# Kernel tuning notes

Measured on AMD Instinct MI355X. Metric: run time of the kernel, lower is better.

The kernel has to match this reference:

```python
import jax, jax.numpy as jnp
import numpy as np

KEY_BITS = 1024
VALUE_BITS = 1024
CAPACITY = 65536
BATCH = 2048


def setup_inputs() -> dict:
    key = jax.random.key(0)
    kq, kk, kv = jax.random.split(key, 3)
    query = jax.random.randint(kq, (BATCH, KEY_BITS), 0, 2, dtype=jnp.int32)
    keys = jax.random.randint(kk, (CAPACITY, KEY_BITS), 0, 2, dtype=jnp.int32)
    values = jax.random.normal(kv, (CAPACITY, VALUE_BITS), dtype=jnp.float32)
    return {"query": query, "keys": keys, "values": values}


def reference(query, keys, values):
    # Hamming mismatches between 0/1 bit vectors via GEMM:
    #   popcount(q ^ k) = sum(q) + sum(k) - 2 * (q . k)
    qf = query.astype(jnp.float32)                      # [B, key_bits]
    kf = keys.astype(jnp.float32)                       # [C, key_bits]
    dot = jnp.einsum('bk,ck->bc', qf, kf)               # [B, C]
    mismatches = qf.sum(axis=1, keepdims=True) + kf.sum(axis=1)[None, :] - 2.0 * dot
    sim = KEY_BITS - mismatches                         # similarity = key_bits - Hamming dist
    best_idx = jnp.argmax(sim, axis=1)                  # first max, matches strict '>' loop
    return values[best_idx]                             # [B, value_bits]
```

## Files before the change

### kernel.cpp

```cpp
#include <hip/hip_runtime.h>
#include <stdint.h>

typedef int v4i  __attribute__((ext_vector_type(4)));
typedef int v16i __attribute__((ext_vector_type(16)));

#define CAPACITY  65536
#define BATCH     2048
#define KBITS     1024
#define NSTEP     16
#define NBUF      3


__global__ void prep_i8_kernel(const int* __restrict__ in,
                               unsigned char* __restrict__ out8,
                               int* __restrict__ sums) {
    const int row = blockIdx.x, t = threadIdx.x;
    int4 v = reinterpret_cast<const int4*>(in)[(size_t)row * 256 + t];
    uint32_t b = (uint32_t)(v.x & 1)        | ((uint32_t)(v.y & 1) << 8) |
                 ((uint32_t)(v.z & 1) << 16) | ((uint32_t)(v.w & 1) << 24);
    reinterpret_cast<uint32_t*>(out8)[(size_t)row * 256 + t] = b;
    int s = (v.x & 1) + (v.y & 1) + (v.z & 1) + (v.w & 1);
    for (int off = 32; off; off >>= 1) s += __shfl_xor(s, off, 64);
    __shared__ int ws4[4];
    if ((t & 63) == 0) ws4[t >> 6] = s;
    __syncthreads();
    if (t == 0) sums[row] = ws4[0] + ws4[1] + ws4[2] + ws4[3];
}

__global__ void init_best_kernel(uint32_t* __restrict__ best) {
    best[blockIdx.x * 256 + threadIdx.x] = 0xFFFFFFFFu;
}

__device__ __forceinline__ int swz(int idx) { return idx ^ ((idx >> 3) & 7); }

__launch_bounds__(256, 2)
__global__ void gemm_scan_kernel(const unsigned char* __restrict__ qi8,
                                 const unsigned char* __restrict__ ki8,
                                 const int* __restrict__ sumk,
                                 uint32_t* __restrict__ best) {
    __shared__ uint4 sA[NBUF][512];
    __shared__ uint4 sB[NBUF][1024];

    const int t    = threadIdx.x;
    const int lane = t & 63, wid = t >> 6;
    const int wr   = wid >> 1, wc = wid & 1;
    const int ln   = lane & 31, kh = lane >> 5;

    const int b     = blockIdx.x;
    const int slot  = b >> 3;
    const int ntile = (b & 7) * 32 + (slot >> 4);
    const int mtile = slot & 15;
    const int m0 = mtile * 128, n0 = ntile * 256;

    const unsigned char* aSrc[2];
    const unsigned char* bSrc[4];
#pragma unroll
    for (int i = 0; i < 2; ++i) {
        int idx = swz(wid * 128 + i * 64 + lane);
        aSrc[i] = qi8 + (size_t)(m0 + (idx >> 2)) * KBITS + (idx & 3) * 16;
    }
#pragma unroll
    for (int i = 0; i < 4; ++i) {
        int idx = swz(wid * 256 + i * 64 + lane);
        bSrc[i] = ki8 + (size_t)(n0 + (idx >> 2)) * KBITS + (idx & 3) * 16;
    }

    auto STAGE = [&](int buf, int kc) {
#pragma unroll
        for (int i = 0; i < 2; ++i)
            __builtin_amdgcn_global_load_lds(
                (const __attribute__((address_space(1))) void*)(aSrc[i] + kc),
                (__attribute__((address_space(3))) void*)&sA[buf][wid * 128 + i * 64],
                16, 0, 0);
#pragma unroll
        for (int i = 0; i < 4; ++i)
            __builtin_amdgcn_global_load_lds(
                (const __attribute__((address_space(1))) void*)(bSrc[i] + kc),
                (__attribute__((address_space(3))) void*)&sB[buf][wid * 256 + i * 64],
                16, 0, 0);
    };

    int offA[2][2], offB[2][4];
#pragma unroll
    for (int km = 0; km < 2; ++km) {
#pragma unroll
        for (int rt = 0; rt < 2; ++rt)
            offA[km][rt] = swz((wr * 64 + rt * 32 + ln) * 4 + km * 2 + kh);
#pragma unroll
        for (int ct = 0; ct < 4; ++ct)
            offB[km][ct] = swz((wc * 128 + ct * 32 + ln) * 4 + km * 2 + kh);
    }

    v16i acc[2][4];
#pragma unroll
    for (int rt = 0; rt < 2; ++rt)
#pragma unroll
        for (int ct = 0; ct < 4; ++ct)
#pragma unroll
            for (int e = 0; e < 16; ++e) acc[rt][ct][e] = 0;

    STAGE(0, 0);
    STAGE(1, 64);
    asm volatile("s_waitcnt vmcnt(6)" ::: "memory");
    __builtin_amdgcn_s_barrier();

    int buf = 0;
    for (int s = 0; s < NSTEP; ++s) {
        if (s + 2 < NSTEP) {
            int nb = buf + 2; if (nb >= NBUF) nb -= NBUF;
            STAGE(nb, (s + 2) * 64);
        }

        uint4 af[2][2], bf[2][4];
#pragma unroll
        for (int km = 0; km < 2; ++km) {
#pragma unroll
            for (int rt = 0; rt < 2; ++rt) af[km][rt] = sA[buf][offA[km][rt]];
#pragma unroll
            for (int ct = 0; ct < 4; ++ct) bf[km][ct] = sB[buf][offB[km][ct]];
        }
#pragma unroll
        for (int km = 0; km < 2; ++km)
#pragma unroll
            for (int rt = 0; rt < 2; ++rt)
#pragma unroll
                for (int ct = 0; ct < 4; ++ct)
                    acc[rt][ct] = __builtin_amdgcn_mfma_i32_32x32x32_i8(
                        *(v4i*)&af[km][rt], *(v4i*)&bf[km][ct], acc[rt][ct], 0, 0, 0);

        if (s < NSTEP - 1) {
            if (s < NSTEP - 2)
                asm volatile("s_waitcnt vmcnt(6) lgkmcnt(0)" ::: "memory");
            else
                asm volatile("s_waitcnt vmcnt(0) lgkmcnt(0)" ::: "memory");
            __builtin_amdgcn_s_barrier();
        }
        buf = buf + 1 == NBUF ? 0 : buf + 1;
    }

    int sk[4];
#pragma unroll
    for (int ct = 0; ct < 4; ++ct) sk[ct] = sumk[n0 + wc * 128 + ct * 32 + ln];

#pragma unroll
    for (int rt = 0; rt < 2; ++rt) {
#pragma unroll
        for (int r = 0; r < 16; ++r) {
            const int qrow = m0 + wr * 64 + rt * 32 + (r & 3) + 8 * (r >> 2) + 4 * kh;
            uint32_t bmin = 0xFFFFFFFFu;
#pragma unroll
            for (int ct = 0; ct < 4; ++ct) {
                uint32_t dist = (uint32_t)(sk[ct] - 2 * acc[rt][ct][r] + 2048);
                uint32_t col  = (uint32_t)(n0 + wc * 128 + ct * 32 + ln);
                bmin = min(bmin, (dist << 16) | col);
            }
#pragma unroll
            for (int off = 1; off < 32; off <<= 1)
                bmin = min(bmin, (uint32_t)__shfl_xor((int)bmin, off, 64));
            if (ln == 0) atomicMin(&best[qrow], bmin);
        }
    }
}

__global__ void finalize_kernel(const uint32_t* __restrict__ best,
                                const float* __restrict__ values,
                                float* __restrict__ out) {
    const int qy  = blockIdx.x;
    const int idx = (int)(best[qy] & 0xFFFFu);
    const float4* v4 = reinterpret_cast<const float4*>(values) + (size_t)idx * 256;
    float4* o4 = reinterpret_cast<float4*>(out) + (size_t)qy * 256;
    o4[threadIdx.x] = v4[threadIdx.x];
}

#define KCHUNK 256
#define NSPLIT (CAPACITY / KCHUNK)

__device__ __forceinline__ uint32_t pack_word(const int4* __restrict__ p) {
    uint32_t word = 0;
#pragma unroll
    for (int j = 0; j < 8; ++j) {
        int4 v = p[j];
        word |= (uint32_t)(v.x & 1) << (4 * j + 0);
        word |= (uint32_t)(v.y & 1) << (4 * j + 1);
        word |= (uint32_t)(v.z & 1) << (4 * j + 2);
        word |= (uint32_t)(v.w & 1) << (4 * j + 3);
    }
    return word;
}

__global__ void pack_bits_kernel(const int* __restrict__ in,
                                 uint32_t* __restrict__ out, int nwords) {
    int w = blockIdx.x * blockDim.x + threadIdx.x;
    if (w >= nwords) return;
    out[w] = pack_word(reinterpret_cast<const int4*>(in) + (size_t)w * 8);
}

__launch_bounds__(256, 4)
__global__ void scan_kernel(const uint32_t* __restrict__ qpack,
                            const uint32_t* __restrict__ kpack,
                            uint32_t* __restrict__ best) {
    const int t      = threadIdx.x;
    const int lane   = t & 63;
    const int wid    = t >> 6;
    const int ksplit = blockIdx.x & (NSPLIT - 1);
    const int qgb    = blockIdx.x >> 8;
    const int query  = qgb * 256 + wid * 64 + lane;

    uint32_t q[32];
    const uint4* qp4 = reinterpret_cast<const uint4*>(qpack + (size_t)query * 32);
#pragma unroll
    for (int j = 0; j < 8; ++j) {
        uint4 v = qp4[j];
        q[4 * j + 0] = v.x; q[4 * j + 1] = v.y;
        q[4 * j + 2] = v.z; q[4 * j + 3] = v.w;
    }
    uint32_t bst = 0xFFFFFFFFu;
    const int k0 = ksplit * KCHUNK;
#pragma unroll 2
    for (int k = k0; k < k0 + KCHUNK; ++k) {
        const uint4* kw4 = reinterpret_cast<const uint4*>(kpack + (size_t)k * 32);
        uint32_t dist = 0;
#pragma unroll
        for (int j = 0; j < 8; ++j) {
            uint4 kv = kw4[j];
            dist += __popc(kv.x ^ q[4 * j + 0]);
            dist += __popc(kv.y ^ q[4 * j + 1]);
            dist += __popc(kv.z ^ q[4 * j + 2]);
            dist += __popc(kv.w ^ q[4 * j + 3]);
        }
        bst = min(bst, (dist << 16) | (uint32_t)k);
    }
    atomicMin(&best[query], bst);
}

extern "C" void kernel_launch(void* const* d_in, const int* in_sizes, int n_in,
                              void* d_out, int out_size, void* d_ws, size_t ws_size,
                              hipStream_t stream) {
    const int*   query  = (const int*)d_in[0];
    const int*   keys   = (const int*)d_in[1];
    const float* values = (const float*)d_in[2];
    float*       out    = (float*)d_out;
    char* ws = (char*)d_ws;

    const size_t need = 2097152ULL + 67108864ULL + 262144ULL + 8192ULL + 8192ULL;
    if (ws_size >= need) {
        unsigned char* qi8 = (unsigned char*)ws;
        unsigned char* ki8 = (unsigned char*)(ws + 2097152);
        int* sumk = (int*)(ws + 2097152 + 67108864);
        int* sumq = (int*)(ws + 2097152 + 67108864 + 262144);
        uint32_t* best = (uint32_t*)(ws + 2097152 + 67108864 + 262144 + 8192);

        init_best_kernel<<<BATCH / 256, 256, 0, stream>>>(best);
        prep_i8_kernel<<<BATCH,    256, 0, stream>>>(query, qi8, sumq);
        prep_i8_kernel<<<CAPACITY, 256, 0, stream>>>(keys,  ki8, sumk);
        gemm_scan_kernel<<<16 * 256, 256, 0, stream>>>(qi8, ki8, sumk, best);
        finalize_kernel<<<BATCH, 256, 0, stream>>>(best, values, out);
    } else {
        uint32_t* qpack = (uint32_t*)ws;
        uint32_t* kpack = (uint32_t*)(ws + 262144);
        uint32_t* best  = (uint32_t*)(ws + 262144 + 8388608);

        init_best_kernel<<<BATCH / 256, 256, 0, stream>>>(best);
        pack_bits_kernel<<<BATCH * 32 / 256, 256, 0, stream>>>(query, qpack, BATCH * 32);
        pack_bits_kernel<<<CAPACITY * 32 / 256, 256, 0, stream>>>(keys, kpack, CAPACITY * 32);
        scan_kernel<<<8 * NSPLIT, 256, 0, stream>>>(qpack, kpack, best);
        finalize_kernel<<<BATCH, 256, 0, stream>>>(best, values, out);
    }
}
```

Baseline: 273.3 us.

## Load query operand directly from transposed global layout, bypassing LDS staging

A new prep kernel writes the int8 query bits in a K-chunk-major transposed layout, so each lane can fetch its MFMA A fragments with coalesced 16-byte global loads straight into registers. A is no longer staged in LDS, which removes its async copies and LDS reads and shrinks the shared-memory footprint. The MFMA blocks are also wrapped in s_setprio to raise wave priority during compute, and the unused query sums are dropped. The cost is that A global-load latency now sits in each step without multi-buffering, and these loads share the vmcnt counter with the B prefetches, which can make the waits stall longer.

```diff
diff --git a/kernel.cpp b/kernel.cpp
--- a/kernel.cpp
+++ b/kernel.cpp
@@ -10,6 +10,15 @@
 #define NSTEP     16
 #define NBUF      3
 
+
+__global__ void prep_qT_kernel(const int* __restrict__ in,
+                               uint32_t* __restrict__ outT) {
+    const int row = blockIdx.x, t = threadIdx.x;
+    int4 v = reinterpret_cast<const int4*>(in)[(size_t)row * 256 + t];
+    uint32_t b = (uint32_t)(v.x & 1)        | ((uint32_t)(v.y & 1) << 8) |
+                 ((uint32_t)(v.z & 1) << 16) | ((uint32_t)(v.w & 1) << 24);
+    outT[(size_t)(t >> 2) * (BATCH * 4) + (size_t)row * 4 + (t & 3)] = b;
+}
 
 __global__ void prep_i8_kernel(const int* __restrict__ in,
                                unsigned char* __restrict__ out8,
@@ -34,11 +43,10 @@
 __device__ __forceinline__ int swz(int idx) { return idx ^ ((idx >> 3) & 7); }
 
 __launch_bounds__(256, 2)
-__global__ void gemm_scan_kernel(const unsigned char* __restrict__ qi8,
+__global__ void gemm_scan_kernel(const uint4* __restrict__ aT4,
                                  const unsigned char* __restrict__ ki8,
                                  const int* __restrict__ sumk,
                                  uint32_t* __restrict__ best) {
-    __shared__ uint4 sA[NBUF][512];
     __shared__ uint4 sB[NBUF][1024];
 
     const int t    = threadIdx.x;
@@ -52,26 +60,13 @@
     const int mtile = slot & 15;
     const int m0 = mtile * 128, n0 = ntile * 256;
 
-    const unsigned char* aSrc[2];
     const unsigned char* bSrc[4];
-#pragma unroll
-    for (int i = 0; i < 2; ++i) {
-        int idx = swz(wid * 128 + i * 64 + lane);
-        aSrc[i] = qi8 + (size_t)(m0 + (idx >> 2)) * KBITS + (idx & 3) * 16;
-    }
 #pragma unroll
     for (int i = 0; i < 4; ++i) {
         int idx = swz(wid * 256 + i * 64 + lane);
         bSrc[i] = ki8 + (size_t)(n0 + (idx >> 2)) * KBITS + (idx & 3) * 16;
     }
-
-    auto STAGE = [&](int buf, int kc) {
-#pragma unroll
-        for (int i = 0; i < 2; ++i)
-            __builtin_amdgcn_global_load_lds(
-                (const __attribute__((address_space(1))) void*)(aSrc[i] + kc),
-                (__attribute__((address_space(3))) void*)&sA[buf][wid * 128 + i * 64],
-                16, 0, 0);
+    auto STAGE_B = [&](int buf, int kc) {
 #pragma unroll
         for (int i = 0; i < 4; ++i)
             __builtin_amdgcn_global_load_lds(
@@ -80,16 +75,14 @@
                 16, 0, 0);
     };
 
-    int offA[2][2], offB[2][4];
-#pragma unroll
-    for (int km = 0; km < 2; ++km) {
-#pragma unroll
-        for (int rt = 0; rt < 2; ++rt)
-            offA[km][rt] = swz((wr * 64 + rt * 32 + ln) * 4 + km * 2 + kh);
+    int offB[2][4];
+#pragma unroll
+    for (int km = 0; km < 2; ++km)
 #pragma unroll
         for (int ct = 0; ct < 4; ++ct)
             offB[km][ct] = swz((wc * 128 + ct * 32 + ln) * 4 + km * 2 + kh);
-    }
+
+    const int mbase = m0 + wr * 64 + ln;
 
     v16i acc[2][4];
 #pragma unroll
@@ -99,38 +92,52 @@
 #pragma unroll
             for (int e = 0; e < 16; ++e) acc[rt][ct][e] = 0;
 
-    STAGE(0, 0);
-    STAGE(1, 64);
-    asm volatile("s_waitcnt vmcnt(6)" ::: "memory");
+    STAGE_B(0, 0);
+    STAGE_B(1, 64);
+    asm volatile("s_waitcnt vmcnt(4)" ::: "memory");
     __builtin_amdgcn_s_barrier();
 
     int buf = 0;
     for (int s = 0; s < NSTEP; ++s) {
+        uint4 af[2][2];
+#pragma unroll
+        for (int km = 0; km < 2; ++km)
+#pragma unroll
+            for (int rt = 0; rt < 2; ++rt)
+                af[km][rt] = aT4[(size_t)(s * 4 + km * 2 + kh) * BATCH
+                                 + mbase + rt * 32];
+
         if (s + 2 < NSTEP) {
             int nb = buf + 2; if (nb >= NBUF) nb -= NBUF;
-            STAGE(nb, (s + 2) * 64);
-        }
-
-        uint4 af[2][2], bf[2][4];
-#pragma unroll
-        for (int km = 0; km < 2; ++km) {
-#pragma unroll
-            for (int rt = 0; rt < 2; ++rt) af[km][rt] = sA[buf][offA[km][rt]];
+            STAGE_B(nb, (s + 2) * 64);
+        }
+
+        uint4 bf[2][4];
+#pragma unroll
+        for (int km = 0; km < 2; ++km)
 #pragma unroll
             for (int ct = 0; ct < 4; ++ct) bf[km][ct] = sB[buf][offB[km][ct]];
-        }
-#pragma unroll
-        for (int km = 0; km < 2; ++km)
-#pragma unroll
-            for (int rt = 0; rt < 2; ++rt)
-#pragma unroll
-                for (int ct = 0; ct < 4; ++ct)
-                    acc[rt][ct] = __builtin_amdgcn_mfma_i32_32x32x32_i8(
-                        *(v4i*)&af[km][rt], *(v4i*)&bf[km][ct], acc[rt][ct], 0, 0, 0);
+
+        __builtin_amdgcn_s_setprio(1);
+#pragma unroll
+        for (int rt = 0; rt < 2; ++rt)
+#pragma unroll
+            for (int ct = 0; ct < 4; ++ct)
+                acc[rt][ct] = __builtin_amdgcn_mfma_i32_32x32x32_i8(
+                    *(v4i*)&af[0][rt], *(v4i*)&bf[0][ct], acc[rt][ct], 0, 0, 0);
+        __builtin_amdgcn_s_setprio(0);
+        __builtin_amdgcn_s_setprio(1);
+#pragma unroll
+        for (int rt = 0; rt < 2; ++rt)
+#pragma unroll
+            for (int ct = 0; ct < 4; ++ct)
+                acc[rt][ct] = __builtin_amdgcn_mfma_i32_32x32x32_i8(
+                    *(v4i*)&af[1][rt], *(v4i*)&bf[1][ct], acc[rt][ct], 0, 0, 0);
+        __builtin_amdgcn_s_setprio(0);
 
         if (s < NSTEP - 1) {
             if (s < NSTEP - 2)
-                asm volatile("s_waitcnt vmcnt(6) lgkmcnt(0)" ::: "memory");
+                asm volatile("s_waitcnt vmcnt(4) lgkmcnt(0)" ::: "memory");
             else
                 asm volatile("s_waitcnt vmcnt(0) lgkmcnt(0)" ::: "memory");
             __builtin_amdgcn_s_barrier();
@@ -242,18 +249,18 @@
     float*       out    = (float*)d_out;
     char* ws = (char*)d_ws;
 
-    const size_t need = 2097152ULL + 67108864ULL + 262144ULL + 8192ULL + 8192ULL;
+    const size_t need = 2097152ULL + 67108864ULL + 262144ULL + 8192ULL;
     if (ws_size >= need) {
-        unsigned char* qi8 = (unsigned char*)ws;
+        uint32_t* qT  = (uint32_t*)ws;
         unsigned char* ki8 = (unsigned char*)(ws + 2097152);
         int* sumk = (int*)(ws + 2097152 + 67108864);
-        int* sumq = (int*)(ws + 2097152 + 67108864 + 262144);
-        uint32_t* best = (uint32_t*)(ws + 2097152 + 67108864 + 262144 + 8192);
+        uint32_t* best = (uint32_t*)(ws + 2097152 + 67108864 + 262144);
 
         init_best_kernel<<<BATCH / 256, 256, 0, stream>>>(best);
-        prep_i8_kernel<<<BATCH,    256, 0, stream>>>(query, qi8, sumq);
-        prep_i8_kernel<<<CAPACITY, 256, 0, stream>>>(keys,  ki8, sumk);
-        gemm_scan_kernel<<<16 * 256, 256, 0, stream>>>(qi8, ki8, sumk, best);
+        prep_qT_kernel<<<BATCH,    256, 0, stream>>>(query, qT);
+        prep_i8_kernel<<<CAPACITY, 256, 0, stream>>>(keys, ki8, sumk);
+        gemm_scan_kernel<<<16 * 256, 256, 0, stream>>>(
+            reinterpret_cast<const uint4*>(qT), ki8, sumk, best);
         finalize_kernel<<<BATCH, 256, 0, stream>>>(best, values, out);
     } else {
         uint32_t* qpack = (uint32_t*)ws;
```

Measured after the change: 265.3 us, median of 3. 1.03x faster.
